# Optimization experiments

Measured on AMD Instinct MI355X. Metric: run time of the kernel, lower is better.

## Reference

```python
import jax, jax.numpy as jnp
from jax import lax
import numpy as np

B, T, F, H = 1024, 512, 1, 60


def _p(key, shape, scale):
    return jax.random.uniform(key, shape, jnp.float32, -scale, scale)


def setup_inputs() -> dict:
    key = jax.random.key(0)
    ks = jax.random.split(key, 40)
    s = 1.0 / np.sqrt(H)
    d = {
        "inputs": jax.random.normal(ks[0], (B, T, F), jnp.float32),
        "outputs": jax.random.normal(ks[1], (B, T, F), jnp.float32),
        # encoder GRU: 3 layers, PyTorch layout W_ih [3H, in], W_hh [3H, H]
        "eW_ih0": _p(ks[2], (3 * H, F), s), "eW_hh0": _p(ks[3], (3 * H, H), s),
        "eb_ih0": _p(ks[4], (3 * H,), s), "eb_hh0": _p(ks[5], (3 * H,), s),
        "eW_ih1": _p(ks[6], (3 * H, H), s), "eW_hh1": _p(ks[7], (3 * H, H), s),
        "eb_ih1": _p(ks[8], (3 * H,), s), "eb_hh1": _p(ks[9], (3 * H,), s),
        "eW_ih2": _p(ks[10], (3 * H, H), s), "eW_hh2": _p(ks[11], (3 * H, H), s),
        "eb_ih2": _p(ks[12], (3 * H,), s), "eb_hh2": _p(ks[13], (3 * H,), s),
        # decoder GRUCells
        "c1_Wih": _p(ks[14], (3 * H, F), s), "c1_Whh": _p(ks[15], (3 * H, H), s),
        "c1_bih": _p(ks[16], (3 * H,), s), "c1_bhh": _p(ks[17], (3 * H,), s),
        "c2_Wih": _p(ks[18], (3 * H, H), s), "c2_Whh": _p(ks[19], (3 * H, H), s),
        "c2_bih": _p(ks[20], (3 * H,), s), "c2_bhh": _p(ks[21], (3 * H,), s),
        "c3_Wih": _p(ks[22], (3 * H, H), s), "c3_Whh": _p(ks[23], (3 * H, H), s),
        "c3_bih": _p(ks[24], (3 * H,), s), "c3_bhh": _p(ks[25], (3 * H,), s),
        # output linear
        "lin_W": _p(ks[26], (F, H), s), "lin_b": _p(ks[27], (F,), s),
    }
    return d


def gru_step(x, h, Wih, Whh, bih, bhh):
    # PyTorch GRU gate math
    gi = x @ Wih.T + bih  # [B, 3H]
    gh = h @ Whh.T + bhh
    ir, iz, inn = jnp.split(gi, 3, axis=-1)
    hr, hz, hn = jnp.split(gh, 3, axis=-1)
    r = jax.nn.sigmoid(ir + hr)
    z = jax.nn.sigmoid(iz + hz)
    n = jnp.tanh(inn + r * hn)
    return (1.0 - z) * n + z * h


def run_gru_layer(x_tbf, Wih, Whh, bih, bhh):
    h0 = jnp.zeros((x_tbf.shape[1], H), x_tbf.dtype)

    def step(h, xt):
        h2 = gru_step(xt, h, Wih, Whh, bih, bhh)
        return h2, h2

    hT, ys = lax.scan(step, h0, x_tbf)
    return ys, hT


def reference(inputs, outputs,
              eW_ih0, eW_hh0, eb_ih0, eb_hh0,
              eW_ih1, eW_hh1, eb_ih1, eb_hh1,
              eW_ih2, eW_hh2, eb_ih2, eb_hh2,
              c1_Wih, c1_Whh, c1_bih, c1_bhh,
              c2_Wih, c2_Whh, c2_bih, c2_bhh,
              c3_Wih, c3_Whh, c3_bih, c3_bhh,
              lin_W, lin_b):
    # --- encoder: 3-layer GRU (eval mode -> inter-layer dropout is identity)
    x = jnp.swapaxes(inputs, 0, 1)  # [T, B, F]
    ys0, h0T = run_gru_layer(x, eW_ih0, eW_hh0, eb_ih0, eb_hh0)
    ys1, h1T = run_gru_layer(ys0, eW_ih1, eW_hh1, eb_ih1, eb_hh1)
    _, h2T = run_gru_layer(ys1, eW_ih2, eW_hh2, eb_ih2, eb_hh2)
    encoded_vec = jnp.stack([h0T, h1T, h2T])  # [3, B, H]

    # --- decoder: 3 stacked GRUCells per step (dropout identity in eval)
    outs_r = jnp.swapaxes(outputs, 0, 1)  # [T, B, F]
    carry0 = (encoded_vec[2], encoded_vec[1], encoded_vec[0])

    def dec_step(carry, xt):
        h1, h2, h3 = carry
        h1 = gru_step(xt, h1, c1_Wih, c1_Whh, c1_bih, c1_bhh)
        h2 = gru_step(h1, h2, c2_Wih, c2_Whh, c2_bih, c2_bhh)
        h3 = gru_step(h2, h3, c3_Wih, c3_Whh, c3_bih, c3_bhh)
        pred = h3 @ lin_W.T + lin_b  # [B, F]
        return (h1, h2, h3), pred

    _, preds = lax.scan(dec_step, carry0, outs_r)  # [T, B, F]
    predicted = jnp.swapaxes(preds, 0, 1)  # [B, T, F]
    return predicted, jnp.swapaxes(encoded_vec, 0, 1)  # [B, 3, H]
```

## Files before the change

### kernel.cpp

```cpp
#include <hip/hip_runtime.h>
#include <hip/hip_bf16.h>

namespace {

constexpr int B = 1024, T = 512, H = 60, G = 180, NTHR = 192;
constexpr int TT = 8;
constexpr int NT = T / TT;

__device__ __forceinline__ float sigm(float x) { return 1.f / (1.f + __expf(-x)); }
__device__ __forceinline__ float tanh_fast(float x) {
  x = fminf(fmaxf(x, -15.f), 15.f);
  const float e = __expf(-2.f * x);
  return (1.f - e) / (1.f + e);
}

__device__ __forceinline__ float ldcvt(const float* p) { return *p; }
__device__ __forceinline__ float ldcvt(const __hip_bfloat16* p) { return __bfloat162float(*p); }
__device__ __forceinline__ void stcvt(float* p, float v) { *p = v; }
__device__ __forceinline__ void stcvt(__hip_bfloat16* p, float v) { *p = __float2bfloat16(v); }

#define ACCH(i, dst)                                                  \
  {                                                                   \
    const float4 hv = *(const float4*)&h_sh[(i) * 4];                 \
    dst = fmaf(Wh##i.x, hv.x, dst);                                   \
    dst = fmaf(Wh##i.y, hv.y, dst);                                   \
    dst = fmaf(Wh##i.z, hv.z, dst);                                   \
    dst = fmaf(Wh##i.w, hv.w, dst);                                   \
  }
#define ACCH_ALL                                                      \
  ACCH(0, c0) ACCH(1, c1) ACCH(2, c2) ACCH(3, c3)                     \
  ACCH(4, c0) ACCH(5, c1) ACCH(6, c2) ACCH(7, c3)                     \
  ACCH(8, c0) ACCH(9, c1) ACCH(10, c2) ACCH(11, c3)                   \
  ACCH(12, c0) ACCH(13, c1) ACCH(14, c2)

#define LWH_ALL                                                       \
  LWH(0) LWH(1) LWH(2) LWH(3) LWH(4) LWH(5) LWH(6) LWH(7)             \
  LWH(8) LWH(9) LWH(10) LWH(11) LWH(12) LWH(13) LWH(14)

template <typename TS, bool WRITE_YS, bool WRITE_ENC>
__global__ __launch_bounds__(NTHR, 1) void gru_scalar_kernel(
    const float* __restrict__ xscalar,
    const float* __restrict__ Wih,
    const float* __restrict__ Whh,
    const float* __restrict__ bih, const float* __restrict__ bhh,
    const float* __restrict__ h_init,
    TS* __restrict__ ys_out,
    float* __restrict__ enc_out)
{
  const int tid = threadIdx.x;
  const int b = blockIdx.x;

  __shared__ __align__(16) float h_sh[64];
  __shared__ float Ar[60], Az[60], Nn[60], Hn[60];
  __shared__ float xs_seq[T];

  const int rr = (tid < G) ? tid : 0;

  float4 Wh0, Wh1, Wh2, Wh3, Wh4, Wh5, Wh6, Wh7, Wh8, Wh9, Wh10, Wh11, Wh12, Wh13, Wh14;
#define LWH(i) Wh##i = *(const float4*)&Whh[(size_t)rr * H + (i) * 4];
  LWH_ALL
#undef LWH
  const float wih0 = Wih[rr];
  const float bi = bih[rr];
  const float bh = bhh[rr];

  if (tid < H) h_sh[tid] = h_init ? h_init[(size_t)b * G + tid] : 0.f;
  for (int i = tid; i < T; i += NTHR) xs_seq[i] = xscalar[(size_t)b * T + i];
  __syncthreads();

  const int g = tid / H;
  const int j = tid - g * H;

  for (int t = 0; t < T; ++t) {
    if (tid < G) {
      float c0 = bh, c1 = 0.f, c2 = 0.f, c3 = 0.f;
      ACCH_ALL
      const float c = (c0 + c1) + (c2 + c3);
      const float a = fmaf(wih0, xs_seq[t], bi);
      if (g == 0)       Ar[j] = a + c;
      else if (g == 1)  Az[j] = a + c;
      else            { Nn[j] = a; Hn[j] = c; }
    }
    __syncthreads();

    if (tid < H) {
      const float rg = sigm(Ar[tid]);
      const float zg = sigm(Az[tid]);
      const float nv = tanh_fast(fmaf(rg, Hn[tid], Nn[tid]));
      const float hnew = fmaf(zg, h_sh[tid] - nv, nv);
      h_sh[tid] = hnew;
      if constexpr (WRITE_YS)
        stcvt(&ys_out[(size_t)t * B * H + (size_t)b * H + tid], hnew);
    }
    __syncthreads();
  }

  if constexpr (WRITE_ENC) {
    if (tid < H) enc_out[(size_t)b * G + tid] = h_sh[tid];
  }
}

template <typename TS, bool WRITE_YS, bool WRITE_ENC, bool WRITE_PRED>
__global__ __launch_bounds__(NTHR, 1) void gru_vec_kernel(
    const TS* __restrict__ xseq,
    const float* __restrict__ Wih,
    const float* __restrict__ Whh,
    const float* __restrict__ bih, const float* __restrict__ bhh,
    const float* __restrict__ h_init,
    TS* __restrict__ ys_out,
    float* __restrict__ enc_out,
    float* __restrict__ pred_out,
    const float* __restrict__ lin_W,
    const float* __restrict__ lin_b)
{
  const int tid = threadIdx.x;
  const int b = blockIdx.x;

  __shared__ __align__(16) float h_sh[64];
  __shared__ __align__(16) float x_sh[2][TT * H];
  __shared__ float gi_sh[TT][G];
  __shared__ float Ar[60], Az[60], Nn[60], Hn[60];
  __shared__ float pv[64];

  const int rr = (tid < G) ? tid : 0;

  float4 Wh0, Wh1, Wh2, Wh3, Wh4, Wh5, Wh6, Wh7, Wh8, Wh9, Wh10, Wh11, Wh12, Wh13, Wh14;
#define LWH(i) Wh##i = *(const float4*)&Whh[(size_t)rr * H + (i) * 4];
  LWH_ALL
#undef LWH
  const float bi = bih[rr];
  const float bh = bhh[rr];

  float linw = 0.f, linb = 0.f;
  if constexpr (WRITE_PRED) {
    linw = lin_W[tid < H ? tid : 0];
    linb = lin_b[0];
  }

  if (tid < H) h_sh[tid] = h_init ? h_init[(size_t)b * G + tid] : 0.f;

  {
    const int i0 = tid, i1 = tid + NTHR, i2 = tid + 2 * NTHR;
    {
      const int s = i0 / H, hh = i0 - s * H;
      x_sh[0][i0] = ldcvt(&xseq[((size_t)s * B + b) * H + hh]);
    }
    {
      const int s = i1 / H, hh = i1 - s * H;
      x_sh[0][i1] = ldcvt(&xseq[((size_t)s * B + b) * H + hh]);
    }
    if (i2 < TT * H) {
      const int s = i2 / H, hh = i2 - s * H;
      x_sh[0][i2] = ldcvt(&xseq[((size_t)s * B + b) * H + hh]);
    }
  }
  __syncthreads();

  const int g = tid / H;
  const int j = tid - g * H;

  for (int tile = 0; tile < NT; ++tile) {
    const int cur = tile & 1;

    float xr0 = 0.f, xr1 = 0.f, xr2 = 0.f;
    const int i0 = tid, i1 = tid + NTHR, i2 = tid + 2 * NTHR;
    if (tile + 1 < NT) {
      const size_t tb = (size_t)(tile + 1) * TT;
      {
        const int s = i0 / H, hh = i0 - s * H;
        xr0 = ldcvt(&xseq[((tb + s) * B + b) * H + hh]);
      }
      {
        const int s = i1 / H, hh = i1 - s * H;
        xr1 = ldcvt(&xseq[((tb + s) * B + b) * H + hh]);
      }
      if (i2 < TT * H) {
        const int s = i2 / H, hh = i2 - s * H;
        xr2 = ldcvt(&xseq[((tb + s) * B + b) * H + hh]);
      }
    }

    asm volatile("" ::: "memory");

    if (tid < G) {
      float acc[TT];
#pragma unroll
      for (int s = 0; s < TT; ++s) acc[s] = bi;
#pragma unroll
      for (int k = 0; k < H / 4; ++k) {
        const float4 w = *(const float4*)&Wih[(size_t)rr * H + k * 4];
#pragma unroll
        for (int s = 0; s < TT; ++s) {
          const float4 xv = *(const float4*)&x_sh[cur][s * H + k * 4];
          acc[s] = fmaf(w.x, xv.x, acc[s]);
          acc[s] = fmaf(w.y, xv.y, acc[s]);
          acc[s] = fmaf(w.z, xv.z, acc[s]);
          acc[s] = fmaf(w.w, xv.w, acc[s]);
        }
      }
#pragma unroll
      for (int s = 0; s < TT; ++s) gi_sh[s][rr] = acc[s];
    }

    if (tile + 1 < NT) {
      x_sh[cur ^ 1][i0] = xr0;
      x_sh[cur ^ 1][i1] = xr1;
      if (i2 < TT * H) x_sh[cur ^ 1][i2] = xr2;
    }
    __syncthreads();

    for (int s = 0; s < TT; ++s) {
      const int t = tile * TT + s;
      if (tid < G) {
        float c0 = bh, c1 = 0.f, c2 = 0.f, c3 = 0.f;
        ACCH_ALL
        const float c = (c0 + c1) + (c2 + c3);
        const float a = gi_sh[s][rr];
        if (g == 0)       Ar[j] = a + c;
        else if (g == 1)  Az[j] = a + c;
        else            { Nn[j] = a; Hn[j] = c; }
      }
      __syncthreads();

      if (tid < H) {
        const float rg = sigm(Ar[tid]);
        const float zg = sigm(Az[tid]);
        const float nv = tanh_fast(fmaf(rg, Hn[tid], Nn[tid]));
        const float hnew = fmaf(zg, h_sh[tid] - nv, nv);
        h_sh[tid] = hnew;
        if constexpr (WRITE_YS)
          stcvt(&ys_out[(size_t)t * B * H + (size_t)b * H + tid], hnew);
        if constexpr (WRITE_PRED) pv[tid] = hnew * linw;
      }
      __syncthreads();

      if constexpr (WRITE_PRED) {
        if (tid < 64) {
          float v = (tid < H) ? pv[tid] : 0.f;
#pragma unroll
          for (int off = 32; off; off >>= 1) v += __shfl_xor(v, off);
          if (tid == 0) pred_out[(size_t)b * T + t] = v + linb;
        }
      }
    }
  }

  if constexpr (WRITE_ENC) {
    if (tid < H) enc_out[(size_t)b * G + tid] = h_sh[tid];
  }
}

template <typename TS>
void launch_all(const float* inputs, const float* outputs,
                const float* eW_ih0, const float* eW_hh0, const float* eb_ih0, const float* eb_hh0,
                const float* eW_ih1, const float* eW_hh1, const float* eb_ih1, const float* eb_hh1,
                const float* eW_ih2, const float* eW_hh2, const float* eb_ih2, const float* eb_hh2,
                const float* c1_Wih, const float* c1_Whh, const float* c1_bih, const float* c1_bhh,
                const float* c2_Wih, const float* c2_Whh, const float* c2_bih, const float* c2_bhh,
                const float* c3_Wih, const float* c3_Whh, const float* c3_bih, const float* c3_bhh,
                const float* lin_W, const float* lin_b,
                float* pred, float* enc, void* d_ws, hipStream_t stream) {
  const size_t seq = (size_t)T * B * H;
  TS* ws0 = (TS*)d_ws;
  TS* ws1 = ws0 + seq;
  const dim3 grid(B), blk(NTHR);

  gru_scalar_kernel<TS, true, true><<<grid, blk, 0, stream>>>(
      inputs, eW_ih0, eW_hh0, eb_ih0, eb_hh0, nullptr, ws0, enc + 0);
  gru_vec_kernel<TS, true, true, false><<<grid, blk, 0, stream>>>(
      ws0, eW_ih1, eW_hh1, eb_ih1, eb_hh1, nullptr,
      ws1, enc + 60, nullptr, nullptr, nullptr);
  gru_vec_kernel<TS, false, true, false><<<grid, blk, 0, stream>>>(
      ws1, eW_ih2, eW_hh2, eb_ih2, eb_hh2, nullptr,
      nullptr, enc + 120, nullptr, nullptr, nullptr);
  gru_scalar_kernel<TS, true, false><<<grid, blk, 0, stream>>>(
      outputs, c1_Wih, c1_Whh, c1_bih, c1_bhh, enc + 120, ws0, nullptr);
  gru_vec_kernel<TS, true, false, false><<<grid, blk, 0, stream>>>(
      ws0, c2_Wih, c2_Whh, c2_bih, c2_bhh, enc + 60,
      ws1, nullptr, nullptr, nullptr, nullptr);
  gru_vec_kernel<TS, false, false, true><<<grid, blk, 0, stream>>>(
      ws1, c3_Wih, c3_Whh, c3_bih, c3_bhh, enc + 0,
      nullptr, nullptr, pred, lin_W, lin_b);
}

}

extern "C" void kernel_launch(void* const* d_in, const int* in_sizes, int n_in,
                              void* d_out, int out_size, void* d_ws, size_t ws_size,
                              hipStream_t stream) {
  const float* inputs  = (const float*)d_in[0];
  const float* outputs = (const float*)d_in[1];
  const float* eW_ih0 = (const float*)d_in[2];  const float* eW_hh0 = (const float*)d_in[3];
  const float* eb_ih0 = (const float*)d_in[4];  const float* eb_hh0 = (const float*)d_in[5];
  const float* eW_ih1 = (const float*)d_in[6];  const float* eW_hh1 = (const float*)d_in[7];
  const float* eb_ih1 = (const float*)d_in[8];  const float* eb_hh1 = (const float*)d_in[9];
  const float* eW_ih2 = (const float*)d_in[10]; const float* eW_hh2 = (const float*)d_in[11];
  const float* eb_ih2 = (const float*)d_in[12]; const float* eb_hh2 = (const float*)d_in[13];
  const float* c1_Wih = (const float*)d_in[14]; const float* c1_Whh = (const float*)d_in[15];
  const float* c1_bih = (const float*)d_in[16]; const float* c1_bhh = (const float*)d_in[17];
  const float* c2_Wih = (const float*)d_in[18]; const float* c2_Whh = (const float*)d_in[19];
  const float* c2_bih = (const float*)d_in[20]; const float* c2_bhh = (const float*)d_in[21];
  const float* c3_Wih = (const float*)d_in[22]; const float* c3_Whh = (const float*)d_in[23];
  const float* c3_bih = (const float*)d_in[24]; const float* c3_bhh = (const float*)d_in[25];
  const float* lin_W  = (const float*)d_in[26]; const float* lin_b  = (const float*)d_in[27];

  float* pred = (float*)d_out;
  float* enc  = pred + (size_t)B * T;

  const size_t seq = (size_t)T * B * H;

#define ARGS inputs, outputs, \
    eW_ih0, eW_hh0, eb_ih0, eb_hh0, eW_ih1, eW_hh1, eb_ih1, eb_hh1, \
    eW_ih2, eW_hh2, eb_ih2, eb_hh2, \
    c1_Wih, c1_Whh, c1_bih, c1_bhh, c2_Wih, c2_Whh, c2_bih, c2_bhh, \
    c3_Wih, c3_Whh, c3_bih, c3_bhh, lin_W, lin_b, pred, enc, d_ws, stream

  if (ws_size >= 2 * seq * sizeof(float)) {
    launch_all<float>(ARGS);
  } else {
    launch_all<__hip_bfloat16>(ARGS);
  }
#undef ARGS
}
```

Before: 3.467 ms.

## Split GRU hidden-state dot products across two thread halves in vec kernel

The vectorized GRU kernel now launches 384 threads per block, and each gate row's recurrent and input dot products are split into two K-halves (32 and 28 columns). Partial sums go to shared memory and are added up in the gate-update phase. This shortens the serial per-step FMA chain and cuts per-thread weight registers, aiming to reduce latency on the recurrent critical path. It also drops one barrier per tile and pads shared arrays to 64 columns. The cost is more waves taking part in every per-step barrier and extra shared-memory reads to combine the partials.

```diff
diff --git a/kernel.cpp b/kernel.cpp
--- a/kernel.cpp
+++ b/kernel.cpp
@@ -3,7 +3,9 @@
 
 namespace {
 
-constexpr int B = 1024, T = 512, H = 60, G = 180, NTHR = 192;
+constexpr int B = 1024, T = 512, H = 60, G = 180;
+constexpr int NTHR = 192;
+constexpr int NTHRV = 384;
 constexpr int TT = 8;
 constexpr int NT = T / TT;
 
@@ -27,15 +29,6 @@
     dst = fmaf(Wh##i.z, hv.z, dst);                                   \
     dst = fmaf(Wh##i.w, hv.w, dst);                                   \
   }
-#define ACCH_ALL                                                      \
-  ACCH(0, c0) ACCH(1, c1) ACCH(2, c2) ACCH(3, c3)                     \
-  ACCH(4, c0) ACCH(5, c1) ACCH(6, c2) ACCH(7, c3)                     \
-  ACCH(8, c0) ACCH(9, c1) ACCH(10, c2) ACCH(11, c3)                   \
-  ACCH(12, c0) ACCH(13, c1) ACCH(14, c2)
-
-#define LWH_ALL                                                       \
-  LWH(0) LWH(1) LWH(2) LWH(3) LWH(4) LWH(5) LWH(6) LWH(7)             \
-  LWH(8) LWH(9) LWH(10) LWH(11) LWH(12) LWH(13) LWH(14)
 
 template <typename TS, bool WRITE_YS, bool WRITE_ENC>
 __global__ __launch_bounds__(NTHR, 1) void gru_scalar_kernel(
@@ -58,13 +51,15 @@
 
   float4 Wh0, Wh1, Wh2, Wh3, Wh4, Wh5, Wh6, Wh7, Wh8, Wh9, Wh10, Wh11, Wh12, Wh13, Wh14;
 #define LWH(i) Wh##i = *(const float4*)&Whh[(size_t)rr * H + (i) * 4];
-  LWH_ALL
+  LWH(0) LWH(1) LWH(2) LWH(3) LWH(4) LWH(5) LWH(6) LWH(7)
+  LWH(8) LWH(9) LWH(10) LWH(11) LWH(12) LWH(13) LWH(14)
 #undef LWH
   const float wih0 = Wih[rr];
   const float bi = bih[rr];
   const float bh = bhh[rr];
 
   if (tid < H) h_sh[tid] = h_init ? h_init[(size_t)b * G + tid] : 0.f;
+  if (tid >= H && tid < 64) h_sh[tid] = 0.f;
   for (int i = tid; i < T; i += NTHR) xs_seq[i] = xscalar[(size_t)b * T + i];
   __syncthreads();
 
@@ -74,7 +69,10 @@
   for (int t = 0; t < T; ++t) {
     if (tid < G) {
       float c0 = bh, c1 = 0.f, c2 = 0.f, c3 = 0.f;
-      ACCH_ALL
+      ACCH(0, c0) ACCH(1, c1) ACCH(2, c2) ACCH(3, c3)
+      ACCH(4, c0) ACCH(5, c1) ACCH(6, c2) ACCH(7, c3)
+      ACCH(8, c0) ACCH(9, c1) ACCH(10, c2) ACCH(11, c3)
+      ACCH(12, c0) ACCH(13, c1) ACCH(14, c2)
       const float c = (c0 + c1) + (c2 + c3);
       const float a = fmaf(wih0, xs_seq[t], bi);
       if (g == 0)       Ar[j] = a + c;
@@ -101,7 +99,7 @@
 }
 
 template <typename TS, bool WRITE_YS, bool WRITE_ENC, bool WRITE_PRED>
-__global__ __launch_bounds__(NTHR, 1) void gru_vec_kernel(
+__global__ __launch_bounds__(NTHRV, 1) void gru_vec_kernel(
     const TS* __restrict__ xseq,
     const float* __restrict__ Wih,
     const float* __restrict__ Whh,
@@ -117,19 +115,23 @@
   const int b = blockIdx.x;
 
   __shared__ __align__(16) float h_sh[64];
-  __shared__ __align__(16) float x_sh[2][TT * H];
-  __shared__ float gi_sh[TT][G];
-  __shared__ float Ar[60], Az[60], Nn[60], Hn[60];
+  __shared__ __align__(16) float x_sh[2][TT][64];
+  __shared__ float gip[2][TT][184];
+  __shared__ float cpart[2][3 * 64];
   __shared__ float pv[64];
 
-  const int rr = (tid < G) ? tid : 0;
-
-  float4 Wh0, Wh1, Wh2, Wh3, Wh4, Wh5, Wh6, Wh7, Wh8, Wh9, Wh10, Wh11, Wh12, Wh13, Wh14;
-#define LWH(i) Wh##i = *(const float4*)&Whh[(size_t)rr * H + (i) * 4];
-  LWH_ALL
-#undef LWH
-  const float bi = bih[rr];
-  const float bh = bhh[rr];
+  const bool act = tid < 2 * G;
+  const int hf = (tid >= G) ? 1 : 0;
+  const int r = act ? (tid - hf * G) : 0;
+  const int off = hf * 32;
+
+  float4 Wh0, Wh1, Wh2, Wh3, Wh4, Wh5, Wh6, Wh7;
+#define LWHH(i) Wh##i = *(const float4*)&Whh[(size_t)r * H + off + (i) * 4];
+  LWHH(0) LWHH(1) LWHH(2) LWHH(3) LWHH(4) LWHH(5) LWHH(6)
+#undef LWHH
+  Wh7 = (hf == 0) ? *(const float4*)&Whh[(size_t)r * H + 28] : make_float4(0, 0, 0, 0);
+  const float bi = (hf == 0) ? bih[r] : 0.f;
+  const float bh = (hf == 0) ? bhh[r] : 0.f;
 
   float linw = 0.f, linb = 0.f;
   if constexpr (WRITE_PRED) {
@@ -137,95 +139,99 @@
     linb = lin_b[0];
   }
 
-  if (tid < H) h_sh[tid] = h_init ? h_init[(size_t)b * G + tid] : 0.f;
-
+  if (tid < 64) h_sh[tid] = (tid < H && h_init) ? h_init[(size_t)b * G + tid] : 0.f;
+  if (tid < 2 * TT) {
+    float4* p = (float4*)&x_sh[tid / TT][tid % TT][60];
+    *p = make_float4(0, 0, 0, 0);
+  }
   {
-    const int i0 = tid, i1 = tid + NTHR, i2 = tid + 2 * NTHR;
+    const int e0 = tid, e1 = tid + NTHRV;
     {
-      const int s = i0 / H, hh = i0 - s * H;
-      x_sh[0][i0] = ldcvt(&xseq[((size_t)s * B + b) * H + hh]);
-    }
-    {
-      const int s = i1 / H, hh = i1 - s * H;
-      x_sh[0][i1] = ldcvt(&xseq[((size_t)s * B + b) * H + hh]);
-    }
-    if (i2 < TT * H) {
-      const int s = i2 / H, hh = i2 - s * H;
-      x_sh[0][i2] = ldcvt(&xseq[((size_t)s * B + b) * H + hh]);
+      const int s = e0 / H, hh = e0 - s * H;
+      if (e0 < TT * H) x_sh[0][s][hh] = ldcvt(&xseq[((size_t)s * B + b) * H + hh]);
+    }
+    if (e1 < TT * H) {
+      const int s = e1 / H, hh = e1 - s * H;
+      x_sh[0][s][hh] = ldcvt(&xseq[((size_t)s * B + b) * H + hh]);
     }
   }
   __syncthreads();
 
-  const int g = tid / H;
-  const int j = tid - g * H;
+  const int g = r / H;
+  const int j = r - g * H;
+  const int cidx = hf * 192 + g * 64 + j;
+  float* cp = &((float*)cpart)[cidx];
 
   for (int tile = 0; tile < NT; ++tile) {
-    const int cur = tile & 1;
-
-    float xr0 = 0.f, xr1 = 0.f, xr2 = 0.f;
-    const int i0 = tid, i1 = tid + NTHR, i2 = tid + 2 * NTHR;
+    const int cur = tile & 1, nxt = cur ^ 1;
+
+    float xr0 = 0.f, xr1 = 0.f;
+    const int e0 = tid, e1 = tid + NTHRV;
     if (tile + 1 < NT) {
       const size_t tb = (size_t)(tile + 1) * TT;
-      {
-        const int s = i0 / H, hh = i0 - s * H;
+      if (e0 < TT * H) {
+        const int s = e0 / H, hh = e0 - s * H;
         xr0 = ldcvt(&xseq[((tb + s) * B + b) * H + hh]);
       }
-      {
-        const int s = i1 / H, hh = i1 - s * H;
+      if (e1 < TT * H) {
+        const int s = e1 / H, hh = e1 - s * H;
         xr1 = ldcvt(&xseq[((tb + s) * B + b) * H + hh]);
       }
-      if (i2 < TT * H) {
-        const int s = i2 / H, hh = i2 - s * H;
-        xr2 = ldcvt(&xseq[((tb + s) * B + b) * H + hh]);
-      }
-    }
-
-    asm volatile("" ::: "memory");
-
-    if (tid < G) {
-      float acc[TT];
+    }
+
+    if (act) {
+      float a0 = bi, a1 = bi, a2 = bi, a3 = bi, a4 = bi, a5 = bi, a6 = bi, a7 = bi;
 #pragma unroll
-      for (int s = 0; s < TT; ++s) acc[s] = bi;
-#pragma unroll
-      for (int k = 0; k < H / 4; ++k) {
-        const float4 w = *(const float4*)&Wih[(size_t)rr * H + k * 4];
-#pragma unroll
-        for (int s = 0; s < TT; ++s) {
-          const float4 xv = *(const float4*)&x_sh[cur][s * H + k * 4];
-          acc[s] = fmaf(w.x, xv.x, acc[s]);
-          acc[s] = fmaf(w.y, xv.y, acc[s]);
-          acc[s] = fmaf(w.z, xv.z, acc[s]);
-          acc[s] = fmaf(w.w, xv.w, acc[s]);
+      for (int k = 0; k < 8; ++k) {
+        float4 w = make_float4(0, 0, 0, 0);
+        if (hf == 0 || k < 7) w = *(const float4*)&Wih[(size_t)r * H + off + k * 4];
+#define GX(s, a)                                                      \
+        {                                                             \
+          const float4 xv = *(const float4*)&x_sh[cur][s][off + k * 4];\
+          a = fmaf(w.x, xv.x, a); a = fmaf(w.y, xv.y, a);             \
+          a = fmaf(w.z, xv.z, a); a = fmaf(w.w, xv.w, a);             \
         }
-      }
-#pragma unroll
-      for (int s = 0; s < TT; ++s) gi_sh[s][rr] = acc[s];
+        GX(0, a0) GX(1, a1) GX(2, a2) GX(3, a3)
+        GX(4, a4) GX(5, a5) GX(6, a6) GX(7, a7)
+#undef GX
+      }
+      gip[hf][0][r] = a0; gip[hf][1][r] = a1; gip[hf][2][r] = a2; gip[hf][3][r] = a3;
+      gip[hf][4][r] = a4; gip[hf][5][r] = a5; gip[hf][6][r] = a6; gip[hf][7][r] = a7;
     }
 
     if (tile + 1 < NT) {
-      x_sh[cur ^ 1][i0] = xr0;
-      x_sh[cur ^ 1][i1] = xr1;
-      if (i2 < TT * H) x_sh[cur ^ 1][i2] = xr2;
-    }
-    __syncthreads();
-
+      if (e0 < TT * H) { const int s = e0 / H, hh = e0 - s * H; x_sh[nxt][s][hh] = xr0; }
+      if (e1 < TT * H) { const int s = e1 / H, hh = e1 - s * H; x_sh[nxt][s][hh] = xr1; }
+    }
+
+#pragma unroll 1
     for (int s = 0; s < TT; ++s) {
       const int t = tile * TT + s;
-      if (tid < G) {
-        float c0 = bh, c1 = 0.f, c2 = 0.f, c3 = 0.f;
-        ACCH_ALL
-        const float c = (c0 + c1) + (c2 + c3);
-        const float a = gi_sh[s][rr];
-        if (g == 0)       Ar[j] = a + c;
-        else if (g == 1)  Az[j] = a + c;
-        else            { Nn[j] = a; Hn[j] = c; }
+      if (act) {
+        float c0 = bh, c1 = 0.f;
+#define HC(i, dst)                                                    \
+        {                                                             \
+          const float4 hv = *(const float4*)&h_sh[off + (i) * 4];     \
+          dst = fmaf(Wh##i.x, hv.x, dst); dst = fmaf(Wh##i.y, hv.y, dst); \
+          dst = fmaf(Wh##i.z, hv.z, dst); dst = fmaf(Wh##i.w, hv.w, dst); \
+        }
+        HC(0, c0) HC(1, c1) HC(2, c0) HC(3, c1)
+        HC(4, c0) HC(5, c1) HC(6, c0) HC(7, c1)
+#undef HC
+        *cp = c0 + c1;
       }
       __syncthreads();
 
       if (tid < H) {
-        const float rg = sigm(Ar[tid]);
-        const float zg = sigm(Az[tid]);
-        const float nv = tanh_fast(fmaf(rg, Hn[tid], Nn[tid]));
+        const float pr = gip[0][s][tid]       + gip[1][s][tid]
+                       + cpart[0][tid]        + cpart[1][tid];
+        const float pz = gip[0][s][H + tid]   + gip[1][s][H + tid]
+                       + cpart[0][64 + tid]   + cpart[1][64 + tid];
+        const float pa = gip[0][s][2 * H + tid] + gip[1][s][2 * H + tid];
+        const float pc = cpart[0][128 + tid]  + cpart[1][128 + tid];
+        const float rg = sigm(pr);
+        const float zg = sigm(pz);
+        const float nv = tanh_fast(fmaf(rg, pc, pa));
         const float hnew = fmaf(zg, h_sh[tid] - nv, nv);
         h_sh[tid] = hnew;
         if constexpr (WRITE_YS)
@@ -238,7 +244,7 @@
         if (tid < 64) {
           float v = (tid < H) ? pv[tid] : 0.f;
 #pragma unroll
-          for (int off = 32; off; off >>= 1) v += __shfl_xor(v, off);
+          for (int o = 32; o; o >>= 1) v += __shfl_xor(v, o);
           if (tid == 0) pred_out[(size_t)b * T + t] = v + linb;
         }
       }
@@ -263,22 +269,22 @@
   const size_t seq = (size_t)T * B * H;
   TS* ws0 = (TS*)d_ws;
   TS* ws1 = ws0 + seq;
-  const dim3 grid(B), blk(NTHR);
+  const dim3 grid(B), blk(NTHR), blkv(NTHRV);
 
   gru_scalar_kernel<TS, true, true><<<grid, blk, 0, stream>>>(
       inputs, eW_ih0, eW_hh0, eb_ih0, eb_hh0, nullptr, ws0, enc + 0);
-  gru_vec_kernel<TS, true, true, false><<<grid, blk, 0, stream>>>(
+  gru_vec_kernel<TS, true, true, false><<<grid, blkv, 0, stream>>>(
       ws0, eW_ih1, eW_hh1, eb_ih1, eb_hh1, nullptr,
       ws1, enc + 60, nullptr, nullptr, nullptr);
-  gru_vec_kernel<TS, false, true, false><<<grid, blk, 0, stream>>>(
+  gru_vec_kernel<TS, false, true, false><<<grid, blkv, 0, stream>>>(
       ws1, eW_ih2, eW_hh2, eb_ih2, eb_hh2, nullptr,
       nullptr, enc + 120, nullptr, nullptr, nullptr);
   gru_scalar_kernel<TS, true, false><<<grid, blk, 0, stream>>>(
       outputs, c1_Wih, c1_Whh, c1_bih, c1_bhh, enc + 120, ws0, nullptr);
-  gru_vec_kernel<TS, true, false, false><<<grid, blk, 0, stream>>>(
+  gru_vec_kernel<TS, true, false, false><<<grid, blkv, 0, stream>>>(
       ws0, c2_Wih, c2_Whh, c2_bih, c2_bhh, enc + 60,
       ws1, nullptr, nullptr, nullptr, nullptr);
-  gru_vec_kernel<TS, false, false, true><<<grid, blk, 0, stream>>>(
+  gru_vec_kernel<TS, false, false, true><<<grid, blkv, 0, stream>>>(
       ws1, c3_Wih, c3_Whh, c3_bih, c3_bhh, enc + 0,
       nullptr, nullptr, pred, lin_W, lin_b);
 }
```

New measurement: 12.36 ms. 257% more time.

## Process four batch rows per block with LDS-resident GRU weights

Applied to the files above, without the earlier changes.

The vector GRU kernel now handles four batch rows per block (grid B/4). Both weight matrices live in shared memory with padded rows and are reused across the four rows. The input projection is computed each step together with the recurrent product, instead of being precomputed per tile from global memory. The prediction dot product is moved to spare threads and lagged by one step, which removes the separate shuffle-reduction phase. The intent is to amortise weight traffic and synchronisation over more rows, at the cost of fewer blocks on the GPU and more LDS reads per step.

```diff
diff --git a/kernel.cpp b/kernel.cpp
--- a/kernel.cpp
+++ b/kernel.cpp
@@ -3,9 +3,12 @@
 
 namespace {
 
-constexpr int B = 1024, T = 512, H = 60, G = 180, NTHR = 192;
+constexpr int B = 1024, T = 512, H = 60, G = 180;
+constexpr int NTHR = 192;
+constexpr int NB = 4;
 constexpr int TT = 8;
 constexpr int NT = T / TT;
+constexpr int WSTR = 68;
 
 __device__ __forceinline__ float sigm(float x) { return 1.f / (1.f + __expf(-x)); }
 __device__ __forceinline__ float tanh_fast(float x) {
@@ -27,15 +30,6 @@
     dst = fmaf(Wh##i.z, hv.z, dst);                                   \
     dst = fmaf(Wh##i.w, hv.w, dst);                                   \
   }
-#define ACCH_ALL                                                      \
-  ACCH(0, c0) ACCH(1, c1) ACCH(2, c2) ACCH(3, c3)                     \
-  ACCH(4, c0) ACCH(5, c1) ACCH(6, c2) ACCH(7, c3)                     \
-  ACCH(8, c0) ACCH(9, c1) ACCH(10, c2) ACCH(11, c3)                   \
-  ACCH(12, c0) ACCH(13, c1) ACCH(14, c2)
-
-#define LWH_ALL                                                       \
-  LWH(0) LWH(1) LWH(2) LWH(3) LWH(4) LWH(5) LWH(6) LWH(7)             \
-  LWH(8) LWH(9) LWH(10) LWH(11) LWH(12) LWH(13) LWH(14)
 
 template <typename TS, bool WRITE_YS, bool WRITE_ENC>
 __global__ __launch_bounds__(NTHR, 1) void gru_scalar_kernel(
@@ -58,13 +52,15 @@
 
   float4 Wh0, Wh1, Wh2, Wh3, Wh4, Wh5, Wh6, Wh7, Wh8, Wh9, Wh10, Wh11, Wh12, Wh13, Wh14;
 #define LWH(i) Wh##i = *(const float4*)&Whh[(size_t)rr * H + (i) * 4];
-  LWH_ALL
+  LWH(0) LWH(1) LWH(2) LWH(3) LWH(4) LWH(5) LWH(6) LWH(7)
+  LWH(8) LWH(9) LWH(10) LWH(11) LWH(12) LWH(13) LWH(14)
 #undef LWH
   const float wih0 = Wih[rr];
   const float bi = bih[rr];
   const float bh = bhh[rr];
 
   if (tid < H) h_sh[tid] = h_init ? h_init[(size_t)b * G + tid] : 0.f;
+  if (tid >= H && tid < 64) h_sh[tid] = 0.f;
   for (int i = tid; i < T; i += NTHR) xs_seq[i] = xscalar[(size_t)b * T + i];
   __syncthreads();
 
@@ -74,7 +70,10 @@
   for (int t = 0; t < T; ++t) {
     if (tid < G) {
       float c0 = bh, c1 = 0.f, c2 = 0.f, c3 = 0.f;
-      ACCH_ALL
+      ACCH(0, c0) ACCH(1, c1) ACCH(2, c2) ACCH(3, c3)
+      ACCH(4, c0) ACCH(5, c1) ACCH(6, c2) ACCH(7, c3)
+      ACCH(8, c0) ACCH(9, c1) ACCH(10, c2) ACCH(11, c3)
+      ACCH(12, c0) ACCH(13, c1) ACCH(14, c2)
       const float c = (c0 + c1) + (c2 + c3);
       const float a = fmaf(wih0, xs_seq[t], bi);
       if (g == 0)       Ar[j] = a + c;
@@ -101,7 +100,7 @@
 }
 
 template <typename TS, bool WRITE_YS, bool WRITE_ENC, bool WRITE_PRED>
-__global__ __launch_bounds__(NTHR, 1) void gru_vec_kernel(
+__global__ __launch_bounds__(NTHR, 1) void gru_vec4_kernel(
     const TS* __restrict__ xseq,
     const float* __restrict__ Wih,
     const float* __restrict__ Whh,
@@ -110,144 +109,185 @@
     TS* __restrict__ ys_out,
     float* __restrict__ enc_out,
     float* __restrict__ pred_out,
-    const float* __restrict__ lin_W,
-    const float* __restrict__ lin_b)
+    const float* __restrict__ linW,
+    const float* __restrict__ linb)
 {
   const int tid = threadIdx.x;
-  const int b = blockIdx.x;
-
-  __shared__ __align__(16) float h_sh[64];
-  __shared__ __align__(16) float x_sh[2][TT * H];
-  __shared__ float gi_sh[TT][G];
-  __shared__ float Ar[60], Az[60], Nn[60], Hn[60];
-  __shared__ float pv[64];
+  const int b0 = blockIdx.x * NB;
+
+  __shared__ __align__(16) float wih_l[G][WSTR];
+  __shared__ __align__(16) float whh_l[G][WSTR];
+  __shared__ __align__(16) float x_l[2][TT * NB * H];
+  __shared__ __align__(16) float h_l[NB][WSTR];
+  __shared__ float gates_l[NB][4][64];
+  __shared__ float lw_l[64];
+
+  for (int i = tid; i < G * H; i += NTHR) {
+    const int r = i / H, k = i - r * H;
+    wih_l[r][k] = Wih[i];
+    whh_l[r][k] = Whh[i];
+  }
+  for (int i = tid; i < NB * WSTR; i += NTHR) {
+    const int b = i / WSTR, j = i - b * WSTR;
+    float hv = 0.f;
+    if (j < H && h_init) hv = h_init[(size_t)(b0 + b) * G + j];
+    h_l[b][j] = hv;
+  }
+  float lb = 0.f;
+  if constexpr (WRITE_PRED) {
+    if (tid < H) lw_l[tid] = linW[tid];
+    lb = linb[0];
+  }
 
   const int rr = (tid < G) ? tid : 0;
-
-  float4 Wh0, Wh1, Wh2, Wh3, Wh4, Wh5, Wh6, Wh7, Wh8, Wh9, Wh10, Wh11, Wh12, Wh13, Wh14;
-#define LWH(i) Wh##i = *(const float4*)&Whh[(size_t)rr * H + (i) * 4];
-  LWH_ALL
-#undef LWH
   const float bi = bih[rr];
   const float bh = bhh[rr];
-
-  float linw = 0.f, linb = 0.f;
-  if constexpr (WRITE_PRED) {
-    linw = lin_W[tid < H ? tid : 0];
-    linb = lin_b[0];
-  }
-
-  if (tid < H) h_sh[tid] = h_init ? h_init[(size_t)b * G + tid] : 0.f;
-
+  const int g = rr / H;
+  const int j = rr - g * H;
+
+#define XGADDR(f, t0) ((((size_t)((t0) + (f) / (NB * H)) * B + b0) * H) + ((f) % (NB * H)))
   {
-    const int i0 = tid, i1 = tid + NTHR, i2 = tid + 2 * NTHR;
-    {
-      const int s = i0 / H, hh = i0 - s * H;
-      x_sh[0][i0] = ldcvt(&xseq[((size_t)s * B + b) * H + hh]);
-    }
-    {
-      const int s = i1 / H, hh = i1 - s * H;
-      x_sh[0][i1] = ldcvt(&xseq[((size_t)s * B + b) * H + hh]);
-    }
-    if (i2 < TT * H) {
-      const int s = i2 / H, hh = i2 - s * H;
-      x_sh[0][i2] = ldcvt(&xseq[((size_t)s * B + b) * H + hh]);
+#pragma unroll
+    for (int q = 0; q < 10; ++q) {
+      const int f = q * NTHR + tid;
+      x_l[0][f] = ldcvt(&xseq[XGADDR(f, 0)]);
     }
   }
   __syncthreads();
 
-  const int g = tid / H;
-  const int j = tid - g * H;
-
   for (int tile = 0; tile < NT; ++tile) {
-    const int cur = tile & 1;
-
-    float xr0 = 0.f, xr1 = 0.f, xr2 = 0.f;
-    const int i0 = tid, i1 = tid + NTHR, i2 = tid + 2 * NTHR;
+    const int cur = tile & 1, nxt = cur ^ 1;
+
+    float p0 = 0, p1 = 0, p2 = 0, p3 = 0, p4 = 0, p5 = 0, p6 = 0, p7 = 0, p8 = 0, p9 = 0;
     if (tile + 1 < NT) {
-      const size_t tb = (size_t)(tile + 1) * TT;
-      {
-        const int s = i0 / H, hh = i0 - s * H;
-        xr0 = ldcvt(&xseq[((tb + s) * B + b) * H + hh]);
-      }
-      {
-        const int s = i1 / H, hh = i1 - s * H;
-        xr1 = ldcvt(&xseq[((tb + s) * B + b) * H + hh]);
-      }
-      if (i2 < TT * H) {
-        const int s = i2 / H, hh = i2 - s * H;
-        xr2 = ldcvt(&xseq[((tb + s) * B + b) * H + hh]);
-      }
-    }
-
-    asm volatile("" ::: "memory");
-
-    if (tid < G) {
-      float acc[TT];
-#pragma unroll
-      for (int s = 0; s < TT; ++s) acc[s] = bi;
-#pragma unroll
-      for (int k = 0; k < H / 4; ++k) {
-        const float4 w = *(const float4*)&Wih[(size_t)rr * H + k * 4];
-#pragma unroll
-        for (int s = 0; s < TT; ++s) {
-          const float4 xv = *(const float4*)&x_sh[cur][s * H + k * 4];
-          acc[s] = fmaf(w.x, xv.x, acc[s]);
-          acc[s] = fmaf(w.y, xv.y, acc[s]);
-          acc[s] = fmaf(w.z, xv.z, acc[s]);
-          acc[s] = fmaf(w.w, xv.w, acc[s]);
-        }
-      }
-#pragma unroll
-      for (int s = 0; s < TT; ++s) gi_sh[s][rr] = acc[s];
-    }
-
-    if (tile + 1 < NT) {
-      x_sh[cur ^ 1][i0] = xr0;
-      x_sh[cur ^ 1][i1] = xr1;
-      if (i2 < TT * H) x_sh[cur ^ 1][i2] = xr2;
-    }
-    __syncthreads();
+      const int t0 = (tile + 1) * TT;
+#define PF(q) p##q = ldcvt(&xseq[XGADDR(q * NTHR + tid, t0)]);
+      PF(0) PF(1) PF(2) PF(3) PF(4) PF(5) PF(6) PF(7) PF(8) PF(9)
+#undef PF
+    }
 
     for (int s = 0; s < TT; ++s) {
       const int t = tile * TT + s;
+
       if (tid < G) {
-        float c0 = bh, c1 = 0.f, c2 = 0.f, c3 = 0.f;
-        ACCH_ALL
-        const float c = (c0 + c1) + (c2 + c3);
-        const float a = gi_sh[s][rr];
-        if (g == 0)       Ar[j] = a + c;
-        else if (g == 1)  Az[j] = a + c;
-        else            { Nn[j] = a; Hn[j] = c; }
+        float a0 = bi, a1 = bi, a2 = bi, a3 = bi;
+        float c0 = bh, c1 = bh * 0.f, c2 = 0.f, c3 = 0.f;
+        a0 = bi; a1 = bi; a2 = bi; a3 = bi;
+        c0 = 0.f; c1 = 0.f; c2 = 0.f; c3 = 0.f;
+        const float* xb = &x_l[cur][s * (NB * H)];
+#pragma unroll
+        for (int k = 0; k < 15; ++k) {
+          const float4 wi = *(const float4*)&wih_l[rr][4 * k];
+          const float4 wh = *(const float4*)&whh_l[rr][4 * k];
+          const float4 x0 = *(const float4*)&xb[0 * H + 4 * k];
+          const float4 x1 = *(const float4*)&xb[1 * H + 4 * k];
+          const float4 x2 = *(const float4*)&xb[2 * H + 4 * k];
+          const float4 x3 = *(const float4*)&xb[3 * H + 4 * k];
+          const float4 h0 = *(const float4*)&h_l[0][4 * k];
+          const float4 h1 = *(const float4*)&h_l[1][4 * k];
+          const float4 h2 = *(const float4*)&h_l[2][4 * k];
+          const float4 h3 = *(const float4*)&h_l[3][4 * k];
+          a0 = fmaf(wi.x, x0.x, a0); a0 = fmaf(wi.y, x0.y, a0);
+          a0 = fmaf(wi.z, x0.z, a0); a0 = fmaf(wi.w, x0.w, a0);
+          a1 = fmaf(wi.x, x1.x, a1); a1 = fmaf(wi.y, x1.y, a1);
+          a1 = fmaf(wi.z, x1.z, a1); a1 = fmaf(wi.w, x1.w, a1);
+          a2 = fmaf(wi.x, x2.x, a2); a2 = fmaf(wi.y, x2.y, a2);
+          a2 = fmaf(wi.z, x2.z, a2); a2 = fmaf(wi.w, x2.w, a2);
+          a3 = fmaf(wi.x, x3.x, a3); a3 = fmaf(wi.y, x3.y, a3);
+          a3 = fmaf(wi.z, x3.z, a3); a3 = fmaf(wi.w, x3.w, a3);
+          c0 = fmaf(wh.x, h0.x, c0); c0 = fmaf(wh.y, h0.y, c0);
+          c0 = fmaf(wh.z, h0.z, c0); c0 = fmaf(wh.w, h0.w, c0);
+          c1 = fmaf(wh.x, h1.x, c1); c1 = fmaf(wh.y, h1.y, c1);
+          c1 = fmaf(wh.z, h1.z, c1); c1 = fmaf(wh.w, h1.w, c1);
+          c2 = fmaf(wh.x, h2.x, c2); c2 = fmaf(wh.y, h2.y, c2);
+          c2 = fmaf(wh.z, h2.z, c2); c2 = fmaf(wh.w, h2.w, c2);
+          c3 = fmaf(wh.x, h3.x, c3); c3 = fmaf(wh.y, h3.y, c3);
+          c3 = fmaf(wh.z, h3.z, c3); c3 = fmaf(wh.w, h3.w, c3);
+        }
+        c0 += bh; c1 += bh; c2 += bh; c3 += bh;
+        if (g == 2) {
+          gates_l[0][2][j] = a0; gates_l[0][3][j] = c0;
+          gates_l[1][2][j] = a1; gates_l[1][3][j] = c1;
+          gates_l[2][2][j] = a2; gates_l[2][3][j] = c2;
+          gates_l[3][2][j] = a3; gates_l[3][3][j] = c3;
+        } else {
+          gates_l[0][g][j] = a0 + c0;
+          gates_l[1][g][j] = a1 + c1;
+          gates_l[2][g][j] = a2 + c2;
+          gates_l[3][g][j] = a3 + c3;
+        }
+      } else if constexpr (WRITE_PRED) {
+        if (tid < 184 && t > 0) {
+          const int bq = tid - 180;
+          float s0 = 0, s1 = 0, s2 = 0, s3 = 0;
+#pragma unroll
+          for (int k = 0; k < 15; ++k) {
+            const float4 lw = *(const float4*)&lw_l[4 * k];
+            const float4 hv = *(const float4*)&h_l[bq][4 * k];
+            s0 = fmaf(lw.x, hv.x, s0); s1 = fmaf(lw.y, hv.y, s1);
+            s2 = fmaf(lw.z, hv.z, s2); s3 = fmaf(lw.w, hv.w, s3);
+          }
+          pred_out[(size_t)(b0 + bq) * T + (t - 1)] = (s0 + s1) + (s2 + s3) + lb;
+        }
       }
       __syncthreads();
 
-      if (tid < H) {
-        const float rg = sigm(Ar[tid]);
-        const float zg = sigm(Az[tid]);
-        const float nv = tanh_fast(fmaf(rg, Hn[tid], Nn[tid]));
-        const float hnew = fmaf(zg, h_sh[tid] - nv, nv);
-        h_sh[tid] = hnew;
-        if constexpr (WRITE_YS)
-          stcvt(&ys_out[(size_t)t * B * H + (size_t)b * H + tid], hnew);
-        if constexpr (WRITE_PRED) pv[tid] = hnew * linw;
+      {
+#pragma unroll
+        for (int rep = 0; rep < 2; ++rep) {
+          const int u = tid + rep * NTHR;
+          if (u < NB * H) {
+            const int b = u / H, jj = u - b * H;
+            const float pr = gates_l[b][0][jj];
+            const float pz = gates_l[b][1][jj];
+            const float pa = gates_l[b][2][jj];
+            const float pc = gates_l[b][3][jj];
+            const float rg = sigm(pr), zg = sigm(pz);
+            const float nv = tanh_fast(fmaf(rg, pc, pa));
+            const float hold = h_l[b][jj];
+            const float hnew = fmaf(zg, hold - nv, nv);
+            h_l[b][jj] = hnew;
+            if constexpr (WRITE_YS)
+              stcvt(&ys_out[((size_t)t * B + b0 + b) * H + jj], hnew);
+          }
+        }
+        if (s == TT - 1) {
+          x_l[nxt][0 * NTHR + tid] = p0; x_l[nxt][1 * NTHR + tid] = p1;
+          x_l[nxt][2 * NTHR + tid] = p2; x_l[nxt][3 * NTHR + tid] = p3;
+          x_l[nxt][4 * NTHR + tid] = p4; x_l[nxt][5 * NTHR + tid] = p5;
+          x_l[nxt][6 * NTHR + tid] = p6; x_l[nxt][7 * NTHR + tid] = p7;
+          x_l[nxt][8 * NTHR + tid] = p8; x_l[nxt][9 * NTHR + tid] = p9;
+        }
       }
       __syncthreads();
-
-      if constexpr (WRITE_PRED) {
-        if (tid < 64) {
-          float v = (tid < H) ? pv[tid] : 0.f;
-#pragma unroll
-          for (int off = 32; off; off >>= 1) v += __shfl_xor(v, off);
-          if (tid == 0) pred_out[(size_t)b * T + t] = v + linb;
-        }
+    }
+  }
+
+  if constexpr (WRITE_PRED) {
+    if (tid >= G && tid < G + NB) {
+      const int bq = tid - G;
+      float s0 = 0, s1 = 0, s2 = 0, s3 = 0;
+#pragma unroll
+      for (int k = 0; k < 15; ++k) {
+        const float4 lw = *(const float4*)&lw_l[4 * k];
+        const float4 hv = *(const float4*)&h_l[bq][4 * k];
+        s0 = fmaf(lw.x, hv.x, s0); s1 = fmaf(lw.y, hv.y, s1);
+        s2 = fmaf(lw.z, hv.z, s2); s3 = fmaf(lw.w, hv.w, s3);
       }
-    }
-  }
-
+      pred_out[(size_t)(b0 + bq) * T + (T - 1)] = (s0 + s1) + (s2 + s3) + lb;
+    }
+  }
   if constexpr (WRITE_ENC) {
-    if (tid < H) enc_out[(size_t)b * G + tid] = h_sh[tid];
-  }
+#pragma unroll
+    for (int rep = 0; rep < 2; ++rep) {
+      const int u = tid + rep * NTHR;
+      if (u < NB * H) {
+        const int b = u / H, jj = u - b * H;
+        enc_out[(size_t)(b0 + b) * G + jj] = h_l[b][jj];
+      }
+    }
+  }
+#undef XGADDR
 }
 
 template <typename TS>
@@ -263,22 +303,22 @@
   const size_t seq = (size_t)T * B * H;
   TS* ws0 = (TS*)d_ws;
   TS* ws1 = ws0 + seq;
-  const dim3 grid(B), blk(NTHR);
-
-  gru_scalar_kernel<TS, true, true><<<grid, blk, 0, stream>>>(
+  const dim3 gs(B), gv(B / NB), blk(NTHR);
+
+  gru_scalar_kernel<TS, true, true><<<gs, blk, 0, stream>>>(
       inputs, eW_ih0, eW_hh0, eb_ih0, eb_hh0, nullptr, ws0, enc + 0);
-  gru_vec_kernel<TS, true, true, false><<<grid, blk, 0, stream>>>(
+  gru_vec4_kernel<TS, true, true, false><<<gv, blk, 0, stream>>>(
       ws0, eW_ih1, eW_hh1, eb_ih1, eb_hh1, nullptr,
       ws1, enc + 60, nullptr, nullptr, nullptr);
-  gru_vec_kernel<TS, false, true, false><<<grid, blk, 0, stream>>>(
+  gru_vec4_kernel<TS, false, true, false><<<gv, blk, 0, stream>>>(
       ws1, eW_ih2, eW_hh2, eb_ih2, eb_hh2, nullptr,
       nullptr, enc + 120, nullptr, nullptr, nullptr);
-  gru_scalar_kernel<TS, true, false><<<grid, blk, 0, stream>>>(
+  gru_scalar_kernel<TS, true, false><<<gs, blk, 0, stream>>>(
       outputs, c1_Wih, c1_Whh, c1_bih, c1_bhh, enc + 120, ws0, nullptr);
-  gru_vec_kernel<TS, true, false, false><<<grid, blk, 0, stream>>>(
+  gru_vec4_kernel<TS, true, false, false><<<gv, blk, 0, stream>>>(
       ws0, c2_Wih, c2_Whh, c2_bih, c2_bhh, enc + 60,
       ws1, nullptr, nullptr, nullptr, nullptr);
-  gru_vec_kernel<TS, false, false, true><<<grid, blk, 0, stream>>>(
+  gru_vec4_kernel<TS, false, false, true><<<gv, blk, 0, stream>>>(
       ws1, c3_Wih, c3_Whh, c3_bih, c3_bhh, enc + 0,
       nullptr, nullptr, pred, lin_W, lin_b);
 }
```

Result: slower. 5.424 ms (+56.4%).
